# Performance work log

Measured on AMD Instinct MI355X. Metric: run time of the kernel, lower is better.

The kernel has to match this reference:

```python
import jax, jax.numpy as jnp
import numpy as np

B, S, D, H = 4, 2048, 1024, 16
HD = D // H
TEMP = 0.5
EPS = 1e-5


def setup_inputs() -> dict:
    key = jax.random.key(0)
    ks = jax.random.split(key, 9)
    s = 1.0 / np.sqrt(D)
    # weights stored as [in, out] (equivalent to torch Linear W.T)
    return {
        "x": jax.random.normal(ks[0], (B, S, D), dtype=jnp.float32),
        "Wq": jax.random.uniform(ks[1], (D, D), minval=-s, maxval=s),
        "bq": jnp.zeros((D,), jnp.float32),
        "Wk": jax.random.uniform(ks[2], (D, D), minval=-s, maxval=s),
        "bk": jnp.zeros((D,), jnp.float32),
        "Wv": jax.random.uniform(ks[3], (D, D), minval=-s, maxval=s),
        "bv": jnp.zeros((D,), jnp.float32),
        "Wo": jax.random.uniform(ks[4], (D, D), minval=-s, maxval=s),
        "bo": jnp.zeros((D,), jnp.float32),
        "ln_g": jnp.ones((D,), jnp.float32),
        "ln_b": jnp.zeros((D,), jnp.float32),
    }


def reference(x, Wq, bq, Wk, bk, Wv, bv, Wo, bo, ln_g, ln_b):
    # projections -> [B, H, S, HD]
    def proj(W, b):
        return (x @ W + b).reshape(B, S, H, HD).transpose(0, 2, 1, 3)

    Q, K, V = proj(Wq, bq), proj(Wk, bk), proj(Wv, bv)
    scale = 1.0 / (np.sqrt(HD) * TEMP)
    scores = jnp.einsum("bhqd,bhkd->bhqk", Q, K) * scale  # [B,H,S,S]
    attn = jax.nn.softmax(scores, axis=-1)  # dropout p=0 -> identity
    ctx = jnp.einsum("bhqk,bhkd->bhqd", attn, V)
    ctx = ctx.transpose(0, 2, 1, 3).reshape(B, S, D)
    out = ctx @ Wo + bo
    # layernorm(out + residual)
    h = out + x
    mu = h.mean(axis=-1, keepdims=True)
    var = h.var(axis=-1, keepdims=True)
    out = (h - mu) / jnp.sqrt(var + EPS) * ln_g + ln_b
    avg_attention = attn.mean(axis=1)  # [B, S, S]
    return out, avg_attention
```

## Files before the change

kernel.cpp:

```cpp
#include <hip/hip_runtime.h>

#define DEV static __device__ __forceinline__

typedef float f32x4 __attribute__((ext_vector_type(4)));
typedef __bf16 bf16x8 __attribute__((ext_vector_type(8)));
typedef unsigned short u16x8 __attribute__((ext_vector_type(8)));
typedef unsigned short u16x4 __attribute__((ext_vector_type(4)));
typedef unsigned u32x2 __attribute__((ext_vector_type(2)));

static constexpr float SCALE_LOG2E = 0.25f * 1.4426950408889634f;

DEV unsigned short f2bf(float f) {
  return __builtin_bit_cast(unsigned short, (__bf16)f);
}
DEV unsigned pk2(float a, float b) {
  unsigned short lo = f2bf(a), hi = f2bf(b);
  return (unsigned)lo | ((unsigned)hi << 16);
}
DEV float ex2(float x) { return __builtin_amdgcn_exp2f(x); }
DEV f32x4 fzero() { f32x4 z; z[0] = z[1] = z[2] = z[3] = 0.f; return z; }

DEV void gll16(const void* g, void* l) {
  __builtin_amdgcn_global_load_lds((__attribute__((address_space(1))) void*)g,
                                   (__attribute__((address_space(3))) void*)l, 16, 0, 0);
}
DEV f32x4 mfma16(bf16x8 a, bf16x8 b, f32x4 c) {
  return __builtin_amdgcn_mfma_f32_16x16x32_bf16(a, b, c, 0, 0, 0);
}

__global__ __launch_bounds__(256) void k_cvt_x(const float* __restrict__ x,
                                               unsigned short* __restrict__ xb, int n) {
  int i = (blockIdx.x * 256 + threadIdx.x) * 4;
  if (i < n) {
    f32x4 v = *(const f32x4*)(x + i);
    u16x4 o;
    o[0] = f2bf(v[0]); o[1] = f2bf(v[1]); o[2] = f2bf(v[2]); o[3] = f2bf(v[3]);
    *(u16x4*)(xb + i) = o;
  }
}

__global__ __launch_bounds__(256) void k_cvt_wT(const float* __restrict__ w0,
                                                const float* __restrict__ w1,
                                                const float* __restrict__ w2,
                                                const float* __restrict__ w3,
                                                unsigned short* __restrict__ wt) {
  __shared__ float t[32][33];
  const float* w = blockIdx.z == 0 ? w0 : blockIdx.z == 1 ? w1 : blockIdx.z == 2 ? w2 : w3;
  unsigned short* dst = wt + (size_t)blockIdx.z * 1024 * 1024;
  int n0 = blockIdx.x * 32, k0 = blockIdx.y * 32;
  int tx = threadIdx.x, ty = threadIdx.y;
#pragma unroll
  for (int i = 0; i < 4; ++i)
    t[ty + 8 * i][tx] = w[(size_t)(k0 + ty + 8 * i) * 1024 + n0 + tx];
  __syncthreads();
#pragma unroll
  for (int i = 0; i < 4; ++i)
    dst[(size_t)(n0 + ty + 8 * i) * 1024 + k0 + tx] = f2bf(t[tx][ty + 8 * i]);
}

__global__ __launch_bounds__(256) void k_vT(const unsigned short* __restrict__ V,
                                            unsigned short* __restrict__ Vt) {
  const long base = (long)blockIdx.y * 131072;
  const int s0 = blockIdx.x * 64;
  const int s = threadIdx.x & 63, dg = threadIdx.x >> 6;
  const unsigned short* src = V + base + (long)(s0 + s) * 64 + dg * 16;
  u16x8 a = *(const u16x8*)(src);
  u16x8 b = *(const u16x8*)(src + 8);
  unsigned short* dst = Vt + base + (long)(dg * 16) * 2048 + s0 + s;
#pragma unroll
  for (int i = 0; i < 8; ++i) dst[(long)i * 2048] = a[i];
#pragma unroll
  for (int i = 0; i < 8; ++i) dst[(long)(8 + i) * 2048] = b[i];
}

template <int MODE>
__global__ __launch_bounds__(256) void k_gemm(
    const unsigned short* __restrict__ A, const unsigned short* __restrict__ Bt,
    unsigned short* __restrict__ oq, unsigned short* __restrict__ ok,
    unsigned short* __restrict__ ov, const float* __restrict__ biasq,
    const float* __restrict__ biask, const float* __restrict__ biasv,
    float* __restrict__ outh, const float* __restrict__ xres,
    const float* __restrict__ biaso, int nx) {
  __shared__ unsigned short As[128 * 64];
  __shared__ unsigned short Bs[128 * 64];
  const int tid = threadIdx.x;
  const int w = tid >> 6, ln = tid & 63;
  const int kg = ln >> 4, l15 = ln & 15;
  const int wm = w >> 1, wn = w & 1;
  const int chunk = gridDim.x >> 3;
  const int lin = (blockIdx.x & 7) * chunk + (blockIdx.x >> 3);
  const long arow0 = (long)(lin / nx) * 128;
  const long brow0 = (long)(lin % nx) * 128;

  f32x4 acc[4][4];
#pragma unroll
  for (int m = 0; m < 4; ++m)
#pragma unroll
    for (int n = 0; n < 4; ++n) acc[m][n] = fzero();

  for (int kt = 0; kt < 16; ++kt) {
    __syncthreads();
#pragma unroll
    for (int rnd = 0; rnd < 4; ++rnd) {
      int slot = rnd * 256 + tid;
      int r = slot >> 3, ch = slot & 7;
      int gch = ch ^ (r & 7);
      gll16(A + (arow0 + r) * 1024 + kt * 64 + gch * 8, (char*)As + slot * 16);
      gll16(Bt + (brow0 + r) * 1024 + kt * 64 + gch * 8, (char*)Bs + slot * 16);
    }
    __syncthreads();
#pragma unroll
    for (int kk = 0; kk < 2; ++kk) {
      bf16x8 af[4], bfr[4];
#pragma unroll
      for (int m = 0; m < 4; ++m) {
        int row = wm * 64 + m * 16 + l15;
        int bir = (kk * 64 + kg * 16) ^ ((row & 7) << 4);
        af[m] = *(const bf16x8*)((const char*)As + row * 128 + bir);
      }
#pragma unroll
      for (int n = 0; n < 4; ++n) {
        int row = wn * 64 + n * 16 + l15;
        int bir = (kk * 64 + kg * 16) ^ ((row & 7) << 4);
        bfr[n] = *(const bf16x8*)((const char*)Bs + row * 128 + bir);
      }
#pragma unroll
      for (int m = 0; m < 4; ++m)
#pragma unroll
        for (int n = 0; n < 4; ++n) acc[m][n] = mfma16(af[m], bfr[n], acc[m][n]);
    }
  }

#pragma unroll
  for (int n = 0; n < 4; ++n) {
    int col = (int)brow0 + wn * 64 + n * 16 + l15;
    if (MODE == 0) {
      int which = col >> 10, nn = col & 1023;
      int hh = nn >> 6, dd = nn & 63;
      unsigned short* dst = which == 0 ? oq : which == 1 ? ok : ov;
      const float* bp = which == 0 ? biasq : which == 1 ? biask : biasv;
      float bias = bp[nn];
#pragma unroll
      for (int m = 0; m < 4; ++m) {
        int row0 = (int)arow0 + wm * 64 + m * 16 + kg * 4;
#pragma unroll
        for (int r = 0; r < 4; ++r) {
          int row = row0 + r;
          int bb = row >> 11, ss = row & 2047;
          dst[(((long)(bb * 16 + hh)) * 2048 + ss) * 64 + dd] =
              f2bf(acc[m][n][r] + bias);
        }
      }
    } else {
      float bias = biaso[col];
#pragma unroll
      for (int m = 0; m < 4; ++m) {
        long row0 = arow0 + wm * 64 + m * 16 + kg * 4;
#pragma unroll
        for (int r = 0; r < 4; ++r) {
          long row = row0 + r;
          outh[row * 1024 + col] = acc[m][n][r] + bias + xres[row * 1024 + col];
        }
      }
    }
  }
}

__global__ __launch_bounds__(256, 4) void k_flash(
    const unsigned short* __restrict__ Q, const unsigned short* __restrict__ K,
    const unsigned short* __restrict__ Vtg, unsigned short* __restrict__ ctx,
    float* __restrict__ mrow, float* __restrict__ lrow) {
  __shared__ unsigned short Ks[64 * 64];
  __shared__ unsigned short Vt[64 * 64];
  __shared__ unsigned short Ps[4][16 * 64];
  const int tid = threadIdx.x, w = tid >> 6, ln = tid & 63;
  const int kg = ln >> 4, l15 = ln & 15;
  const int lin = (blockIdx.x & 7) * 256 + (blockIdx.x >> 3);
  const int qt = lin & 31, hh = (lin >> 5) & 15, bb = lin >> 9;
  const long bh = (long)bb * 16 + hh;
  const unsigned short* Qg = Q + bh * 131072;
  const int qrow = qt * 64 + w * 16 + l15;
  const bf16x8 qf0 = *(const bf16x8*)(Qg + (long)qrow * 64 + kg * 8);
  const bf16x8 qf1 = *(const bf16x8*)(Qg + (long)qrow * 64 + 32 + kg * 8);

  const int r0 = tid >> 3, gch = (tid & 7) ^ (r0 & 7);
  const unsigned short* kp0 = K + bh * 131072 + r0 * 64 + gch * 8;
  const unsigned short* kp1 = kp0 + 32 * 64;
  const unsigned short* vp0 = Vtg + bh * 131072 + r0 * 2048 + gch * 8;
  const unsigned short* vp1 = vp0 + 32 * 2048;
  char* kl0 = (char*)Ks + tid * 16;
  char* kl1 = kl0 + 4096;
  char* vl0 = (char*)Vt + tid * 16;
  char* vl1 = vl0 + 4096;

  const int swz = (l15 & 7) << 4;
  int bir[2];
  bir[0] = (kg * 16) ^ swz;
  bir[1] = (64 + kg * 16) ^ swz;
  const char* ksb[4];
  const char* vtb[4];
#pragma unroll
  for (int nf = 0; nf < 4; ++nf) {
    ksb[nf] = (const char*)Ks + (nf * 16 + l15) * 128;
    vtb[nf] = (const char*)Vt + (nf * 16 + l15) * 128;
  }
  char* pw = (char*)Ps[w] + l15 * 128;

  f32x4 oacc[4];
#pragma unroll
  for (int nf = 0; nf < 4; ++nf) oacc[nf] = fzero();
  float m_run = -1e30f, l_run = 0.f;

  for (int kt = 0; kt < 32; ++kt) {
    __syncthreads();
    gll16(kp0, kl0);
    gll16(kp1, kl1);
    gll16(vp0, vl0);
    gll16(vp1, vl1);
    kp0 += 4096; kp1 += 4096; vp0 += 64; vp1 += 64;
    __syncthreads();

    f32x4 st[4];
#pragma unroll
    for (int nf = 0; nf < 4; ++nf) st[nf] = fzero();
#pragma unroll
    for (int kk = 0; kk < 2; ++kk)
#pragma unroll
      for (int nf = 0; nf < 4; ++nf) {
        bf16x8 kb = *(const bf16x8*)(ksb[nf] + bir[kk]);
        st[nf] = mfma16(kb, kk ? qf1 : qf0, st[nf]);
      }

    float mx0 = fmaxf(fmaxf(st[0][0], st[0][1]), fmaxf(st[0][2], st[0][3]));
    float mx1 = fmaxf(fmaxf(st[1][0], st[1][1]), fmaxf(st[1][2], st[1][3]));
    float mx2 = fmaxf(fmaxf(st[2][0], st[2][1]), fmaxf(st[2][2], st[2][3]));
    float mx3 = fmaxf(fmaxf(st[3][0], st[3][1]), fmaxf(st[3][2], st[3][3]));
    float mx = fmaxf(fmaxf(mx0, mx1), fmaxf(mx2, mx3));
    mx = fmaxf(mx, __shfl_xor(mx, 16));
    mx = fmaxf(mx, __shfl_xor(mx, 32));
    mx *= SCALE_LOG2E;
    float mnew = fmaxf(m_run, mx);
    float alpha = ex2(m_run - mnew);
    m_run = mnew;

    float sum = 0.f;
#pragma unroll
    for (int nf = 0; nf < 4; ++nf) {
      float p0 = ex2(st[nf][0] * SCALE_LOG2E - m_run);
      float p1 = ex2(st[nf][1] * SCALE_LOG2E - m_run);
      float p2 = ex2(st[nf][2] * SCALE_LOG2E - m_run);
      float p3 = ex2(st[nf][3] * SCALE_LOG2E - m_run);
      st[nf][0] = p0; st[nf][1] = p1; st[nf][2] = p2; st[nf][3] = p3;
      sum += (p0 + p1) + (p2 + p3);
    }
    sum += __shfl_xor(sum, 16);
    sum += __shfl_xor(sum, 32);
    l_run = l_run * alpha + sum;

#pragma unroll
    for (int nf = 0; nf < 4; ++nf) {
      u32x2 pv2;
      pv2[0] = pk2(st[nf][0], st[nf][1]);
      pv2[1] = pk2(st[nf][2], st[nf][3]);
      *(u32x2*)(pw + ((nf * 32 + kg * 8) ^ swz)) = pv2;
    }

#pragma unroll
    for (int nf = 0; nf < 4; ++nf) oacc[nf] *= alpha;

#pragma unroll
    for (int kk = 0; kk < 2; ++kk) {
      bf16x8 pb = *(const bf16x8*)(pw + bir[kk]);
#pragma unroll
      for (int nf = 0; nf < 4; ++nf) {
        bf16x8 vb = *(const bf16x8*)(vtb[nf] + bir[kk]);
        oacc[nf] = mfma16(vb, pb, oacc[nf]);
      }
    }
  }

  float linv = 1.0f / l_run;
#pragma unroll
  for (int nf = 0; nf < 4; ++nf) {
    u16x4 o;
#pragma unroll
    for (int r = 0; r < 4; ++r) o[r] = f2bf(oacc[nf][r] * linv);
    *(u16x4*)(ctx + ((long)bb * 2048 + qrow) * 1024 + hh * 64 + nf * 16 + kg * 4) = o;
  }
  if (kg == 0) {
    mrow[bh * 2048 + qrow] = m_run;
    lrow[bh * 2048 + qrow] = l_run;
  }
}

__global__ __launch_bounds__(256, 4) void k_avg(
    const unsigned short* __restrict__ Q, const unsigned short* __restrict__ K,
    const float* __restrict__ mrow, const float* __restrict__ lrow,
    float* __restrict__ avg) {
  __shared__ unsigned short Ks[64 * 64];
  const int tid = threadIdx.x, w = tid >> 6, ln = tid & 63;
  const int kg = ln >> 4, l15 = ln & 15;
  const int lin = (blockIdx.x & 7) * 512 + (blockIdx.x >> 3);
  const int kt = lin & 31, qt = (lin >> 5) & 31, bb = lin >> 10;
  const int qrow = qt * 64 + w * 16 + l15;

  const int r0 = tid >> 3, gch = (tid & 7) ^ (r0 & 7);
  const unsigned short* kp0 = K + (long)bb * 16 * 131072 + kt * 4096 + r0 * 64 + gch * 8;
  const unsigned short* kp1 = kp0 + 2048;
  char* kl0 = (char*)Ks + tid * 16;
  char* kl1 = kl0 + 4096;
  const unsigned short* qp = Q + (long)bb * 16 * 131072 + (long)qrow * 64 + kg * 8;
  const float* mp = mrow + (long)bb * 16 * 2048 + qrow;
  const float* lp = lrow + (long)bb * 16 * 2048 + qrow;

  const int swz = (l15 & 7) << 4;
  int bir[2];
  bir[0] = (kg * 16) ^ swz;
  bir[1] = (64 + kg * 16) ^ swz;
  const char* ksb[4];
#pragma unroll
  for (int nf = 0; nf < 4; ++nf) ksb[nf] = (const char*)Ks + (nf * 16 + l15) * 128;

  f32x4 aacc[4];
#pragma unroll
  for (int nf = 0; nf < 4; ++nf) aacc[nf] = fzero();

  for (int hh = 0; hh < 16; ++hh) {
    __syncthreads();
    gll16(kp0, kl0);
    gll16(kp1, kl1);
    bf16x8 q0 = *(const bf16x8*)(qp);
    bf16x8 q1 = *(const bf16x8*)(qp + 32);
    float m = *mp;
    float li = 0.0625f / *lp;
    kp0 += 131072; kp1 += 131072; qp += 131072; mp += 2048; lp += 2048;
    __syncthreads();

    f32x4 st[4];
#pragma unroll
    for (int nf = 0; nf < 4; ++nf) st[nf] = fzero();
#pragma unroll
    for (int kk = 0; kk < 2; ++kk)
#pragma unroll
      for (int nf = 0; nf < 4; ++nf) {
        bf16x8 kb = *(const bf16x8*)(ksb[nf] + bir[kk]);
        st[nf] = mfma16(kb, kk ? q1 : q0, st[nf]);
      }
#pragma unroll
    for (int nf = 0; nf < 4; ++nf)
#pragma unroll
      for (int r = 0; r < 4; ++r)
        aacc[nf][r] += ex2(st[nf][r] * SCALE_LOG2E - m) * li;
  }
#pragma unroll
  for (int nf = 0; nf < 4; ++nf)
    *(f32x4*)(avg + ((long)bb * 2048 + qrow) * 2048 + kt * 64 + nf * 16 + kg * 4) =
        aacc[nf];
}

__global__ __launch_bounds__(256) void k_ln(float* __restrict__ io,
                                            const float* __restrict__ g,
                                            const float* __restrict__ bvec) {
  __shared__ float red[8];
  long row = blockIdx.x;
  float* p = io + row * 1024;
  int tid = threadIdx.x;
  f32x4 v = *(const f32x4*)(p + tid * 4);
  float s = v[0] + v[1] + v[2] + v[3];
  float ss = v[0] * v[0] + v[1] * v[1] + v[2] * v[2] + v[3] * v[3];
#pragma unroll
  for (int m = 1; m < 64; m <<= 1) {
    s += __shfl_xor(s, m);
    ss += __shfl_xor(ss, m);
  }
  int w = tid >> 6;
  if ((tid & 63) == 0) { red[w * 2] = s; red[w * 2 + 1] = ss; }
  __syncthreads();
  s = red[0] + red[2] + red[4] + red[6];
  ss = red[1] + red[3] + red[5] + red[7];
  float mu = s * (1.0f / 1024.0f);
  float var = ss * (1.0f / 1024.0f) - mu * mu;
  float rs = rsqrtf(var + 1e-5f);
  f32x4 o;
#pragma unroll
  for (int i = 0; i < 4; ++i) {
    int c = tid * 4 + i;
    o[i] = (v[i] - mu) * rs * g[c] + bvec[c];
  }
  *(f32x4*)(p + tid * 4) = o;
}

extern "C" void kernel_launch(void* const* d_in, const int* in_sizes, int n_in,
                              void* d_out, int out_size, void* d_ws, size_t ws_size,
                              hipStream_t stream) {
  (void)in_sizes; (void)n_in; (void)out_size; (void)ws_size;
  const float* x  = (const float*)d_in[0];
  const float* Wq = (const float*)d_in[1];
  const float* bq = (const float*)d_in[2];
  const float* Wk = (const float*)d_in[3];
  const float* bk = (const float*)d_in[4];
  const float* Wv = (const float*)d_in[5];
  const float* bv = (const float*)d_in[6];
  const float* Wo = (const float*)d_in[7];
  const float* bo = (const float*)d_in[8];
  const float* lg = (const float*)d_in[9];
  const float* lb = (const float*)d_in[10];
  float* out = (float*)d_out;
  float* avg = out + (long)8192 * 1024;

  char* ws = (char*)d_ws;
  unsigned short* xb  = (unsigned short*)(ws);
  unsigned short* vtg = (unsigned short*)(ws);
  unsigned short* wt  = (unsigned short*)(ws + ((size_t)16 << 20));
  unsigned short* Qb  = (unsigned short*)(ws + ((size_t)24 << 20));
  unsigned short* Kb  = (unsigned short*)(ws + ((size_t)40 << 20));
  unsigned short* Vb  = (unsigned short*)(ws + ((size_t)56 << 20));
  unsigned short* ctx = (unsigned short*)(ws + ((size_t)72 << 20));
  float* mrow = (float*)(ws + ((size_t)88 << 20));
  float* lrow = (float*)(ws + ((size_t)88 << 20) + ((size_t)1 << 19));

  k_cvt_x<<<dim3(8192), dim3(256), 0, stream>>>(x, xb, 8192 * 1024);
  k_cvt_wT<<<dim3(32, 32, 4), dim3(32, 8), 0, stream>>>(Wq, Wk, Wv, Wo, wt);
  k_gemm<0><<<dim3(1536), dim3(256), 0, stream>>>(
      xb, wt, Qb, Kb, Vb, bq, bk, bv, nullptr, nullptr, nullptr, 24);
  k_vT<<<dim3(32, 64), dim3(256), 0, stream>>>(Vb, vtg);
  k_flash<<<dim3(2048), dim3(256), 0, stream>>>(Qb, Kb, vtg, ctx, mrow, lrow);
  k_avg<<<dim3(4096), dim3(256), 0, stream>>>(Qb, Kb, mrow, lrow, avg);
  k_gemm<1><<<dim3(512), dim3(256), 0, stream>>>(
      ctx, wt + (size_t)3 * 1024 * 1024, nullptr, nullptr, nullptr, nullptr, nullptr,
      nullptr, out, x, bo, 8);
  k_ln<<<dim3(8192), dim3(256), 0, stream>>>(out, lg, lb);
}
```

Measured before the change: 465.8 us.

## Double-buffer K/V LDS tiles in flash and avg-attention kernels

```diff
diff --git a/kernel.cpp b/kernel.cpp
--- a/kernel.cpp
+++ b/kernel.cpp
@@ -170,8 +170,8 @@
     const unsigned short* __restrict__ Q, const unsigned short* __restrict__ K,
     const unsigned short* __restrict__ Vtg, unsigned short* __restrict__ ctx,
     float* __restrict__ mrow, float* __restrict__ lrow) {
-  __shared__ unsigned short Ks[64 * 64];
-  __shared__ unsigned short Vt[64 * 64];
+  __shared__ unsigned short Ks[2][64 * 64];
+  __shared__ unsigned short Vt[2][64 * 64];
   __shared__ unsigned short Ps[4][16 * 64];
   const int tid = threadIdx.x, w = tid >> 6, ln = tid & 63;
   const int kg = ln >> 4, l15 = ln & 15;
@@ -184,14 +184,21 @@
   const bf16x8 qf1 = *(const bf16x8*)(Qg + (long)qrow * 64 + 32 + kg * 8);
 
   const int r0 = tid >> 3, gch = (tid & 7) ^ (r0 & 7);
-  const unsigned short* kp0 = K + bh * 131072 + r0 * 64 + gch * 8;
-  const unsigned short* kp1 = kp0 + 32 * 64;
-  const unsigned short* vp0 = Vtg + bh * 131072 + r0 * 2048 + gch * 8;
-  const unsigned short* vp1 = vp0 + 32 * 2048;
-  char* kl0 = (char*)Ks + tid * 16;
-  char* kl1 = kl0 + 4096;
-  char* vl0 = (char*)Vt + tid * 16;
-  char* vl1 = vl0 + 4096;
+  const unsigned short* Kbase = K + bh * 131072 + r0 * 64 + gch * 8;
+  const unsigned short* Vbase = Vtg + bh * 131072 + r0 * 2048 + gch * 8;
+  char* kl = (char*)Ks + tid * 16;
+  char* vl = (char*)Vt + tid * 16;
+
+  auto STAGE = [&](int kt, int b) {
+    const unsigned short* kp = Kbase + kt * 4096;
+    const unsigned short* vp = Vbase + kt * 64;
+    char* kd = kl + b * 8192;
+    char* vd = vl + b * 8192;
+    gll16(kp, kd);
+    gll16(kp + 2048, kd + 4096);
+    gll16(vp, vd);
+    gll16(vp + 65536, vd + 4096);
+  };
 
   const int swz = (l15 & 7) << 4;
   int bir[2];
@@ -211,14 +218,13 @@
   for (int nf = 0; nf < 4; ++nf) oacc[nf] = fzero();
   float m_run = -1e30f, l_run = 0.f;
 
+  STAGE(0, 0);
+  __syncthreads();
+  int cur = 0;
+
   for (int kt = 0; kt < 32; ++kt) {
-    __syncthreads();
-    gll16(kp0, kl0);
-    gll16(kp1, kl1);
-    gll16(vp0, vl0);
-    gll16(vp1, vl1);
-    kp0 += 4096; kp1 += 4096; vp0 += 64; vp1 += 64;
-    __syncthreads();
+    if (kt < 31) STAGE(kt + 1, cur ^ 1);
+    const int co = cur << 13;
 
     f32x4 st[4];
 #pragma unroll
@@ -227,7 +233,7 @@
     for (int kk = 0; kk < 2; ++kk)
 #pragma unroll
       for (int nf = 0; nf < 4; ++nf) {
-        bf16x8 kb = *(const bf16x8*)(ksb[nf] + bir[kk]);
+        bf16x8 kb = *(const bf16x8*)(ksb[nf] + co + bir[kk]);
         st[nf] = mfma16(kb, kk ? qf1 : qf0, st[nf]);
       }
 
@@ -273,10 +279,12 @@
       bf16x8 pb = *(const bf16x8*)(pw + bir[kk]);
 #pragma unroll
       for (int nf = 0; nf < 4; ++nf) {
-        bf16x8 vb = *(const bf16x8*)(vtb[nf] + bir[kk]);
+        bf16x8 vb = *(const bf16x8*)(vtb[nf] + co + bir[kk]);
         oacc[nf] = mfma16(vb, pb, oacc[nf]);
       }
     }
+    __syncthreads();
+    cur ^= 1;
   }
 
   float linv = 1.0f / l_run;
@@ -297,7 +305,7 @@
     const unsigned short* __restrict__ Q, const unsigned short* __restrict__ K,
     const float* __restrict__ mrow, const float* __restrict__ lrow,
     float* __restrict__ avg) {
-  __shared__ unsigned short Ks[64 * 64];
+  __shared__ unsigned short Ks[2][64 * 64];
   const int tid = threadIdx.x, w = tid >> 6, ln = tid & 63;
   const int kg = ln >> 4, l15 = ln & 15;
   const int lin = (blockIdx.x & 7) * 512 + (blockIdx.x >> 3);
@@ -305,10 +313,16 @@
   const int qrow = qt * 64 + w * 16 + l15;
 
   const int r0 = tid >> 3, gch = (tid & 7) ^ (r0 & 7);
-  const unsigned short* kp0 = K + (long)bb * 16 * 131072 + kt * 4096 + r0 * 64 + gch * 8;
-  const unsigned short* kp1 = kp0 + 2048;
-  char* kl0 = (char*)Ks + tid * 16;
-  char* kl1 = kl0 + 4096;
+  const unsigned short* Kbase =
+      K + (long)bb * 16 * 131072 + kt * 4096 + r0 * 64 + gch * 8;
+  char* kl = (char*)Ks + tid * 16;
+  auto STAGE = [&](int h, int b) {
+    const unsigned short* kp = Kbase + (long)h * 131072;
+    char* kd = kl + b * 8192;
+    gll16(kp, kd);
+    gll16(kp + 2048, kd + 4096);
+  };
+
   const unsigned short* qp = Q + (long)bb * 16 * 131072 + (long)qrow * 64 + kg * 8;
   const float* mp = mrow + (long)bb * 16 * 2048 + qrow;
   const float* lp = lrow + (long)bb * 16 * 2048 + qrow;
@@ -325,16 +339,25 @@
 #pragma unroll
   for (int nf = 0; nf < 4; ++nf) aacc[nf] = fzero();
 
+  bf16x8 q0 = *(const bf16x8*)(qp);
+  bf16x8 q1 = *(const bf16x8*)(qp + 32);
+  float m = *mp;
+  float li = 0.0625f / *lp;
+  STAGE(0, 0);
+  __syncthreads();
+  int cur = 0;
+
   for (int hh = 0; hh < 16; ++hh) {
-    __syncthreads();
-    gll16(kp0, kl0);
-    gll16(kp1, kl1);
-    bf16x8 q0 = *(const bf16x8*)(qp);
-    bf16x8 q1 = *(const bf16x8*)(qp + 32);
-    float m = *mp;
-    float li = 0.0625f / *lp;
-    kp0 += 131072; kp1 += 131072; qp += 131072; mp += 2048; lp += 2048;
-    __syncthreads();
+    bf16x8 qn0 = q0, qn1 = q1;
+    float mn = m, lin_ = li;
+    if (hh < 15) {
+      STAGE(hh + 1, cur ^ 1);
+      qn0 = *(const bf16x8*)(qp + (long)(hh + 1) * 131072);
+      qn1 = *(const bf16x8*)(qp + (long)(hh + 1) * 131072 + 32);
+      mn = mp[(hh + 1) * 2048];
+      lin_ = 0.0625f / lp[(hh + 1) * 2048];
+    }
+    const int co = cur << 13;
 
     f32x4 st[4];
 #pragma unroll
@@ -343,7 +366,7 @@
     for (int kk = 0; kk < 2; ++kk)
 #pragma unroll
       for (int nf = 0; nf < 4; ++nf) {
-        bf16x8 kb = *(const bf16x8*)(ksb[nf] + bir[kk]);
+        bf16x8 kb = *(const bf16x8*)(ksb[nf] + co + bir[kk]);
         st[nf] = mfma16(kb, kk ? q1 : q0, st[nf]);
       }
 #pragma unroll
@@ -351,6 +374,10 @@
 #pragma unroll
       for (int r = 0; r < 4; ++r)
         aacc[nf][r] += ex2(st[nf][r] * SCALE_LOG2E - m) * li;
+
+    __syncthreads();
+    cur ^= 1;
+    q0 = qn0; q1 = qn1; m = mn; li = lin_;
   }
 #pragma unroll
   for (int nf = 0; nf < 4; ++nf)
```

Measured after the change: 469.0 us. About the same (+0.7%).
